# Kernel tuning notes

Hardware: AMD Instinct MI355X
Metric: run time of the kernel (lower is better)

## Reference

```python
import jax, jax.numpy as jnp
import numpy as np

B, S, HID = 1, 2048, 1024
HQ, HKV, D = 16, 8, 64
W = 64          # causal window size (includes self at offset 0)
K = 128         # total neighbors per query: W window + (K-W) random rewires


def setup_inputs() -> dict:
    key = jax.random.key(0)
    ks = jax.random.split(key, 8)
    hidden_states = jax.random.normal(ks[0], (B, S, HID), jnp.float32)
    sc = HID ** -0.5
    q_w = jax.random.normal(ks[1], (HQ * D, HID), jnp.float32) * sc
    k_w = jax.random.normal(ks[2], (HKV * D, HID), jnp.float32) * sc
    v_w = jax.random.normal(ks[3], (HKV * D, HID), jnp.float32) * sc
    o_w = jax.random.normal(ks[4], (HQ * D, HID), jnp.float32).T * sc  # [HID, HQ*D] -> stored as [HID, HQ*D]? keep [HID, HQ*D]
    o_w = jax.random.normal(ks[4], (HID, HQ * D), jnp.float32) * sc
    edge_bias = jax.random.normal(ks[5], (4,), jnp.float32) * 0.1
    # neighbor indices: per kv-head, per query position.
    pos = jnp.arange(S)
    win = pos[:, None] - jnp.arange(W)[None, :]                    # [S, W], offset 0 == self
    win = jnp.broadcast_to(win[None], (HKV, S, W))
    rew = jax.random.randint(ks[6], (HKV, S, K - W), 0, S)         # random rewire edges
    neigh_idx = jnp.concatenate([win, rew], axis=-1).astype(jnp.int32)  # [HKV, S, K]
    edge_type = jnp.concatenate([
        jnp.full((HKV, S, W), 1, jnp.int32),       # 'window'
        jnp.full((HKV, S, K - W), 3, jnp.int32),   # 'rewire'
    ], axis=-1)
    return {
        'hidden_states': hidden_states, 'q_w': q_w, 'k_w': k_w, 'v_w': v_w,
        'o_w': o_w, 'edge_bias': edge_bias, 'neigh_idx': neigh_idx,
        'edge_type': edge_type,
    }


def reference(hidden_states, q_w, k_w, v_w, o_w, edge_bias, neigh_idx, edge_type):
    b, s, _ = hidden_states.shape
    hkv, _, kk = neigh_idx.shape
    hq = q_w.shape[0] // (k_w.shape[0] // hkv)
    d = k_w.shape[0] // hkv
    hq = q_w.shape[0] // d
    g = hq // hkv
    scaling = d ** -0.5

    # projections (nn.Linear: x @ W.T)
    q = (hidden_states @ q_w.T).reshape(b, s, hq, d).transpose(0, 2, 1, 3)    # [B,HQ,S,D]
    k = (hidden_states @ k_w.T).reshape(b, s, hkv, d).transpose(0, 2, 1, 3)   # [B,HKV,S,D]
    v = (hidden_states @ v_w.T).reshape(b, s, hkv, d).transpose(0, 2, 1, 3)

    # causal neighbor mask + safe clamp (mirrors _causal_neighbor_mask / _safe_neighbor_idx)
    pos = jnp.arange(s)
    mask = (neigh_idx >= 0) & (neigh_idx < s) & (neigh_idx <= pos[None, :, None])  # [HKV,S,K]
    safe = jnp.clip(neigh_idx, 0, s - 1)

    # gather K/V at neighbor indices: [B,HKV,S,K,D]
    h_idx = jnp.arange(hkv)[:, None, None]
    k_g = k[:, h_idx, safe, :]
    v_g = v[:, h_idx, safe, :]

    # GQA: group query heads over kv heads
    qg = q.reshape(b, hkv, g, s, d)
    scores = jnp.einsum('bhgsd,bhskd->bhgsk', qg, k_g) * scaling              # [B,HKV,G,S,K]
    scores = scores + edge_bias[edge_type][None, :, None, :, :]
    neg = jnp.finfo(scores.dtype).min
    scores = jnp.where(mask[None, :, None, :, :], scores, neg)
    attn = jax.nn.softmax(scores, axis=-1)

    out = jnp.einsum('bhgsk,bhskd->bhgsd', attn, v_g)                         # [B,HKV,G,S,D]
    out = out.reshape(b, hq, s, d).transpose(0, 2, 1, 3).reshape(b, s, hq * d)
    return out @ o_w.T                                                        # [B,S,HID]
```

## Files before the change

kernel.cpp:

```cpp
#include <hip/hip_runtime.h>
#include <hip/hip_bf16.h>

#define S_LEN 2048
#define HIDDEN 1024

typedef __attribute__((ext_vector_type(4))) float f32x4;
typedef __attribute__((ext_vector_type(8))) _Float16 f16x8;
typedef __attribute__((ext_vector_type(2))) _Float16 f16x2;
typedef __attribute__((ext_vector_type(2))) __fp16 fp16x2;
typedef unsigned short u16;
typedef unsigned int u32;

typedef const __attribute__((address_space(1))) unsigned int as1_u32;
typedef __attribute__((address_space(3))) unsigned int as3_u32;

__device__ __forceinline__ u16 f2h(float f) {
  union { _Float16 h; u16 u; } c; c.h = (_Float16)f; return c.u;
}
__device__ __forceinline__ f16x2 u2h2(u32 u) {
  union { u32 x; f16x2 h; } c; c.x = u; return c.h;
}
__device__ __forceinline__ float fdot2(u32 a, u32 b, float c) {
#if __has_builtin(__builtin_amdgcn_fdot2)
  return __builtin_amdgcn_fdot2(u2h2(a), u2h2(b), c, false);
#else
  f16x2 ha = u2h2(a), hb = u2h2(b);
  return fmaf((float)ha.x, (float)hb.x, fmaf((float)ha.y, (float)hb.y, c));
#endif
}
__device__ __forceinline__ u32 pkrtz(float a, float b) {
#if __has_builtin(__builtin_amdgcn_cvt_pkrtz)
  union { fp16x2 h; u32 u; } c;
  c.h = __builtin_amdgcn_cvt_pkrtz(a, b);
  return c.u;
#else
  union { f16x2 h; u32 u; } c;
  c.h.x = (_Float16)a; c.h.y = (_Float16)b;
  return c.u;
#endif
}
__device__ __forceinline__ u32 alignbit16(u32 hi, u32 lo) {
#if __has_builtin(__builtin_amdgcn_alignbit)
  return __builtin_amdgcn_alignbit(hi, lo, 16);
#else
  return (hi << 16) | (lo >> 16);
#endif
}

__global__ __launch_bounds__(256) void cvt_all(
    const float* __restrict__ h, const float* __restrict__ qw,
    const float* __restrict__ kw, const float* __restrict__ vw,
    const float* __restrict__ ow, u16* __restrict__ hb, u16* __restrict__ qwb,
    u16* __restrict__ kwb, u16* __restrict__ vwb, u16* __restrict__ owb) {
  const int b = blockIdx.x;
  const float* src; u16* dst; int base;
  if (b < 2048)      { src = h;  dst = hb;  base = b; }
  else if (b < 3072) { src = qw; dst = qwb; base = b - 2048; }
  else if (b < 3584) { src = kw; dst = kwb; base = b - 3072; }
  else if (b < 4096) { src = vw; dst = vwb; base = b - 3584; }
  else               { src = ow; dst = owb; base = b - 4096; }
  const int i = base * 256 + threadIdx.x;
  const float4 v = ((const float4*)src)[i];
  ushort4 r;
  r.x = f2h(v.x); r.y = f2h(v.y); r.z = f2h(v.z); r.w = f2h(v.w);
  ((ushort4*)dst)[i] = r;
}

template <int BM, bool OUT_F16>
__device__ __forceinline__ void gemm_core(
    u16* __restrict__ As, u16* __restrict__ Bs,
    const u16* __restrict__ A, const u16* __restrict__ W, void* __restrict__ Cv,
    int Kd, int ldc, int mtile, int ntile) {
  constexpr int MF = BM / 32;
  const int tid = threadIdx.x;
  const int lane = tid & 63;
  const int wave = tid >> 6;
  const int wr = wave >> 1, wc = wave & 1;
  f32x4 acc[MF][4] = {};
  const int m0 = mtile * BM, n0 = ntile * 128;
  const int nk = Kd >> 5;

  auto stage = [&](int buf, int kt) {
    u16* Ad = As + buf * (BM * 32);
    u16* Bd = Bs + buf * (128 * 32);
#pragma unroll
    for (int i = 0; i < BM / 64; ++i) {
      const int e = (i * 256 + tid) * 8;
      const int r = e >> 5, c = e & 31;
      __builtin_amdgcn_global_load_lds(
          (as1_u32*)(A + (size_t)(m0 + r) * Kd + kt * 32 + c), (as3_u32*)(Ad + e), 16, 0, 0);
    }
#pragma unroll
    for (int i = 0; i < 2; ++i) {
      const int e = (i * 256 + tid) * 8;
      const int r = e >> 5, c = e & 31;
      __builtin_amdgcn_global_load_lds(
          (as1_u32*)(W + (size_t)(n0 + r) * Kd + kt * 32 + c), (as3_u32*)(Bd + e), 16, 0, 0);
    }
  };

  stage(0, 0);
  __syncthreads();
  int cur = 0;
  for (int kt = 0; kt < nk; ++kt) {
    if (kt + 1 < nk) stage(cur ^ 1, kt + 1);
    const u16* Ac = As + cur * (BM * 32);
    const u16* Bc = Bs + cur * (128 * 32);
    f16x8 af[MF], bfr[4];
#pragma unroll
    for (int mi = 0; mi < MF; ++mi)
      af[mi] = *(const f16x8*)(Ac + (wr * (BM / 2) + mi * 16 + (lane & 15)) * 32 + (lane >> 4) * 8);
#pragma unroll
    for (int ni = 0; ni < 4; ++ni)
      bfr[ni] = *(const f16x8*)(Bc + (wc * 64 + ni * 16 + (lane & 15)) * 32 + (lane >> 4) * 8);
#pragma unroll
    for (int mi = 0; mi < MF; ++mi)
#pragma unroll
      for (int ni = 0; ni < 4; ++ni)
        acc[mi][ni] = __builtin_amdgcn_mfma_f32_16x16x32_f16(af[mi], bfr[ni], acc[mi][ni], 0, 0, 0);
    __syncthreads();
    cur ^= 1;
  }

#pragma unroll
  for (int mi = 0; mi < MF; ++mi) {
#pragma unroll
    for (int ni = 0; ni < 4; ++ni) {
      const int row0 = m0 + wr * (BM / 2) + mi * 16 + (lane >> 4) * 4;
      const int col = n0 + wc * 64 + ni * 16 + (lane & 15);
#pragma unroll
      for (int r = 0; r < 4; ++r) {
        if (OUT_F16)
          ((u16*)Cv)[(size_t)(row0 + r) * ldc + col] = f2h(acc[mi][ni][r]);
        else
          ((float*)Cv)[(size_t)(row0 + r) * ldc + col] = acc[mi][ni][r];
      }
    }
  }
}

__global__ __launch_bounds__(256, 2) void qkv_gemm(
    const u16* __restrict__ hb, const u16* __restrict__ qwb,
    const u16* __restrict__ kwb, const u16* __restrict__ vwb,
    u16* __restrict__ Qb, u16* __restrict__ Kb, u16* __restrict__ Vb) {
  __shared__ u16 As[2 * 128 * 32];
  __shared__ u16 Bs[2 * 128 * 32];
  const int nt = blockIdx.x, mt = blockIdx.y;
  if (nt < 8)       gemm_core<128, true>(As, Bs, hb, qwb, Qb, HIDDEN, 1024, mt, nt);
  else if (nt < 12) gemm_core<128, true>(As, Bs, hb, kwb, Kb, HIDDEN, 512, mt, nt - 8);
  else              gemm_core<128, true>(As, Bs, hb, vwb, Vb, HIDDEN, 512, mt, nt - 12);
}

__global__ __launch_bounds__(256, 2) void o_gemm(
    const u16* __restrict__ attnb, const u16* __restrict__ owb,
    float* __restrict__ out) {
  __shared__ u16 As[2 * 64 * 32];
  __shared__ u16 Bs[2 * 128 * 32];
  gemm_core<64, false>(As, Bs, attnb, owb, out, HIDDEN, 1024, blockIdx.y, blockIdx.x);
}

#define WIN_ROWS 72
#define WIN_ELEMS (WIN_ROWS * 64)
#define VT_LD 41
__global__ __launch_bounds__(256) void attn_kernel(
    const u16* __restrict__ Qb, const u16* __restrict__ Kb,
    const u16* __restrict__ Vb, const int* __restrict__ neigh,
    const float* __restrict__ ebias, u16* __restrict__ attnb) {
  __shared__ u16 kwin[WIN_ELEMS];
  __shared__ u32 vwinT[64 * VT_LD];
  __shared__ u32 park[4][192];

  const int tid = threadIdx.x;
  const int lane = tid & 63;
  const int wv = tid >> 6;
  const int h = blockIdx.y;
  const int s0 = blockIdx.x * 4;
  const int s = s0 + wv;

  const u16* Kp = Kb + h * 64;
  const u16* Vp = Vb + h * 64;

  const int iB = neigh[((size_t)h * S_LEN + s) * 128 + 64 + lane];
  const bool okB = (iB >= 0) && (iB <= s);
  const int gB = min(max(iB, 0), S_LEN - 1);
  const bool okA = lane <= s;

  const u16* krp = Kp + (size_t)gB * 512;
  uint4 krreg[8];
#pragma unroll
  for (int t = 0; t < 8; ++t) krreg[t] = *(const uint4*)(krp + t * 8);

  const int chunk = (lane & 7) ^ (lane >> 3);
#pragma unroll
  for (int gg = 0; gg < 2; ++gg) {
    const int g = wv + gg * 4;
    const int r_lds = g * 8 + (lane >> 3);
    const int row = min(max(s0 - 63 + r_lds, 0), S_LEN - 1);
    __builtin_amdgcn_global_load_lds(
        (as1_u32*)(Kp + (size_t)row * 512 + chunk * 8),
        (as3_u32*)(kwin + g * 512 + lane * 8), 16, 0, 0);
  }
  if (wv == 0) {
    const int g = 8;
    const int r_lds = g * 8 + (lane >> 3);
    const int row = min(max(s0 - 63 + r_lds, 0), S_LEN - 1);
    __builtin_amdgcn_global_load_lds(
        (as1_u32*)(Kp + (size_t)row * 512 + chunk * 8),
        (as3_u32*)(kwin + g * 512 + lane * 8), 16, 0, 0);
  }

#pragma unroll 3
  for (int t = 0; t < 9; ++t) {
    const int k = wv + 4 * t;
    const int i0r = 2 * k;
    const int g0 = min(max(s0 - 63 + i0r, 0), S_LEN - 1);
    const int g1 = min(max(s0 - 62 + i0r, 0), S_LEN - 1);
    const u32 w0 = Vp[(size_t)g0 * 512 + lane];
    const u32 w1 = Vp[(size_t)g1 * 512 + lane];
    vwinT[lane * VT_LD + k] = (w1 << 16) | w0;
  }

  __syncthreads();

  const u16* qp = Qb + (size_t)s * 1024 + h * 128;
  const int rW = wv + 63 - lane;
  const u16* kwrow = kwin + rW * 64;
  const int rw7 = rW & 7;
  float sA0 = 0.f, sA1 = 0.f, sB0 = 0.f, sB1 = 0.f;
#pragma unroll
  for (int t = 0; t < 8; ++t) {
    const uint4 kw = *(const uint4*)(kwrow + ((t ^ rw7) << 3));
    const uint4 kr = krreg[t];
    const uint4 qa = *(const uint4*)(qp + t * 8);
    const uint4 qb = *(const uint4*)(qp + 64 + t * 8);
    sA0 = fdot2(kw.x, qa.x, sA0); sA0 = fdot2(kw.y, qa.y, sA0);
    sA0 = fdot2(kw.z, qa.z, sA0); sA0 = fdot2(kw.w, qa.w, sA0);
    sA1 = fdot2(kw.x, qb.x, sA1); sA1 = fdot2(kw.y, qb.y, sA1);
    sA1 = fdot2(kw.z, qb.z, sA1); sA1 = fdot2(kw.w, qb.w, sA1);
    sB0 = fdot2(kr.x, qa.x, sB0); sB0 = fdot2(kr.y, qa.y, sB0);
    sB0 = fdot2(kr.z, qa.z, sB0); sB0 = fdot2(kr.w, qa.w, sB0);
    sB1 = fdot2(kr.x, qb.x, sB1); sB1 = fdot2(kr.y, qb.y, sB1);
    sB1 = fdot2(kr.z, qb.z, sB1); sB1 = fdot2(kr.w, qb.w, sB1);
  }

  const float NEG = -1e30f;
  const float SC = 0.125f;
  const float ebW = ebias[1];
  const float ebR = ebias[3];
  sA0 = okA ? fmaf(sA0, SC, ebW) : NEG;
  sA1 = okA ? fmaf(sA1, SC, ebW) : NEG;
  sB0 = okB ? fmaf(sB0, SC, ebR) : NEG;
  sB1 = okB ? fmaf(sB1, SC, ebR) : NEG;

  float m0 = fmaxf(sA0, sB0), m1 = fmaxf(sA1, sB1);
#pragma unroll
  for (int off = 32; off; off >>= 1) {
    m0 = fmaxf(m0, __shfl_xor(m0, off));
    m1 = fmaxf(m1, __shfl_xor(m1, off));
  }
  float eA0 = __expf(sA0 - m0), eB0 = __expf(sB0 - m0);
  float eA1 = __expf(sA1 - m1), eB1 = __expf(sB1 - m1);
  float d0 = eA0 + eB0, d1 = eA1 + eB1;
#pragma unroll
  for (int off = 32; off; off >>= 1) {
    d0 += __shfl_xor(d0, off);
    d1 += __shfl_xor(d1, off);
  }
  const float rc0 = 1.0f / d0, rc1 = 1.0f / d1;

  u32* pb = park[wv];
  int* ib = (int*)(park[wv] + 128);
  const float pA0 = eA0 * rc0, pA1 = eA1 * rc1;
  const float pB0 = eB0 * rc0, pB1 = eB1 * rc1;
  const float hA0 = __shfl_xor(pA0, 1), hA1 = __shfl_xor(pA1, 1);
  const float hB0 = __shfl_xor(pB0, 1), hB1 = __shfl_xor(pB1, 1);
  ib[lane] = gB;
  if (!(lane & 1)) {
    uint4 pk;
    pk.x = pkrtz(hA0, pA0);
    pk.y = pkrtz(hA1, pA1);
    pk.z = pkrtz(pB0, hB0);
    pk.w = pkrtz(pB1, hB1);
    *(uint4*)(pb + (lane >> 1) * 4) = pk;
  }
  asm volatile("s_waitcnt lgkmcnt(0)" ::: "memory");

  float a0 = 0.f, a1 = 0.f;
  const u32* vtr = vwinT + lane * VT_LD;
  const int keven = (wv >> 1) + 31;
  const int kodd = ((wv + 63) >> 1);
#pragma unroll 4
  for (int m = 0; m < 32; ++m) {
    const uint4 pp = *(const uint4*)(pb + m * 4);
    const int2 rB = *(const int2*)(ib + m * 2);
    u32 wpair;
    if ((wv & 1) == 0) {
      wpair = vtr[keven - m];
    } else {
      const u32 lo = vtr[kodd - 1 - m];
      const u32 hi = vtr[kodd - m];
      wpair = alignbit16(hi, lo);
    }
    const u32 b0 = Vp[(size_t)rB.x * 512 + lane];
    const u32 b1 = Vp[(size_t)rB.y * 512 + lane];
    const u32 bpair = (b1 << 16) | b0;
    a0 = fdot2(wpair, pp.x, a0);
    a1 = fdot2(wpair, pp.y, a1);
    a0 = fdot2(bpair, pp.z, a0);
    a1 = fdot2(bpair, pp.w, a1);
  }

  u16* op = attnb + (size_t)s * 1024 + h * 128;
  op[lane] = f2h(a0);
  op[64 + lane] = f2h(a1);
}

extern "C" void kernel_launch(void* const* d_in, const int* in_sizes, int n_in,
                              void* d_out, int out_size, void* d_ws, size_t ws_size,
                              hipStream_t stream) {
  const float* hidden = (const float*)d_in[0];
  const float* q_w = (const float*)d_in[1];
  const float* k_w = (const float*)d_in[2];
  const float* v_w = (const float*)d_in[3];
  const float* o_w = (const float*)d_in[4];
  const float* ebias = (const float*)d_in[5];
  const int* neigh = (const int*)d_in[6];
  float* out = (float*)d_out;

  char* ws = (char*)d_ws;
  u16* hb    = (u16*)(ws + (0ull << 20));
  u16* qwb   = (u16*)(ws + (4ull << 20));
  u16* kwb   = (u16*)(ws + (6ull << 20));
  u16* vwb   = (u16*)(ws + (7ull << 20));
  u16* owb   = (u16*)(ws + (8ull << 20));
  u16* Qb    = (u16*)(ws + (10ull << 20));
  u16* Kb    = (u16*)(ws + (14ull << 20));
  u16* Vb    = (u16*)(ws + (16ull << 20));
  u16* attnb = (u16*)(ws + (18ull << 20));

  cvt_all<<<5120, 256, 0, stream>>>(hidden, q_w, k_w, v_w, o_w,
                                    hb, qwb, kwb, vwb, owb);
  qkv_gemm<<<dim3(16, 16), 256, 0, stream>>>(hb, qwb, kwb, vwb, Qb, Kb, Vb);
  attn_kernel<<<dim3(512, 8), 256, 0, stream>>>(Qb, Kb, Vb, neigh, ebias, attnb);
  o_gemm<<<dim3(8, 32), 256, 0, stream>>>(attnb, owb, out);
}
```

Measured before the change: 95.48 us.

## Drop LDS window staging in attention; read window K/V directly from global

```diff
diff --git a/kernel.cpp b/kernel.cpp
--- a/kernel.cpp
+++ b/kernel.cpp
@@ -37,13 +37,6 @@
   union { f16x2 h; u32 u; } c;
   c.h.x = (_Float16)a; c.h.y = (_Float16)b;
   return c.u;
-#endif
-}
-__device__ __forceinline__ u32 alignbit16(u32 hi, u32 lo) {
-#if __has_builtin(__builtin_amdgcn_alignbit)
-  return __builtin_amdgcn_alignbit(hi, lo, 16);
-#else
-  return (hi << 16) | (lo >> 16);
 #endif
 }
 
@@ -159,78 +152,35 @@
   gemm_core<64, false>(As, Bs, attnb, owb, out, HIDDEN, 1024, blockIdx.y, blockIdx.x);
 }
 
-#define WIN_ROWS 72
-#define WIN_ELEMS (WIN_ROWS * 64)
-#define VT_LD 41
 __global__ __launch_bounds__(256) void attn_kernel(
     const u16* __restrict__ Qb, const u16* __restrict__ Kb,
     const u16* __restrict__ Vb, const int* __restrict__ neigh,
     const float* __restrict__ ebias, u16* __restrict__ attnb) {
-  __shared__ u16 kwin[WIN_ELEMS];
-  __shared__ u32 vwinT[64 * VT_LD];
   __shared__ u32 park[4][192];
 
   const int tid = threadIdx.x;
   const int lane = tid & 63;
   const int wv = tid >> 6;
   const int h = blockIdx.y;
-  const int s0 = blockIdx.x * 4;
-  const int s = s0 + wv;
+  const int su = __builtin_amdgcn_readfirstlane(blockIdx.x * 4 + wv);
 
   const u16* Kp = Kb + h * 64;
   const u16* Vp = Vb + h * 64;
 
-  const int iB = neigh[((size_t)h * S_LEN + s) * 128 + 64 + lane];
-  const bool okB = (iB >= 0) && (iB <= s);
+  const int iB = neigh[((size_t)h * S_LEN + su) * 128 + 64 + lane];
+  const bool okB = (iB >= 0) && (iB <= su);
   const int gB = min(max(iB, 0), S_LEN - 1);
-  const bool okA = lane <= s;
-
+  const bool okA = lane <= su;
+  const int gA = max(su - lane, 0);
+
+  const u16* qp = Qb + (size_t)su * 1024 + h * 128;
+  const u16* kwp = Kp + (size_t)gA * 512;
   const u16* krp = Kp + (size_t)gB * 512;
-  uint4 krreg[8];
-#pragma unroll
-  for (int t = 0; t < 8; ++t) krreg[t] = *(const uint4*)(krp + t * 8);
-
-  const int chunk = (lane & 7) ^ (lane >> 3);
-#pragma unroll
-  for (int gg = 0; gg < 2; ++gg) {
-    const int g = wv + gg * 4;
-    const int r_lds = g * 8 + (lane >> 3);
-    const int row = min(max(s0 - 63 + r_lds, 0), S_LEN - 1);
-    __builtin_amdgcn_global_load_lds(
-        (as1_u32*)(Kp + (size_t)row * 512 + chunk * 8),
-        (as3_u32*)(kwin + g * 512 + lane * 8), 16, 0, 0);
-  }
-  if (wv == 0) {
-    const int g = 8;
-    const int r_lds = g * 8 + (lane >> 3);
-    const int row = min(max(s0 - 63 + r_lds, 0), S_LEN - 1);
-    __builtin_amdgcn_global_load_lds(
-        (as1_u32*)(Kp + (size_t)row * 512 + chunk * 8),
-        (as3_u32*)(kwin + g * 512 + lane * 8), 16, 0, 0);
-  }
-
-#pragma unroll 3
-  for (int t = 0; t < 9; ++t) {
-    const int k = wv + 4 * t;
-    const int i0r = 2 * k;
-    const int g0 = min(max(s0 - 63 + i0r, 0), S_LEN - 1);
-    const int g1 = min(max(s0 - 62 + i0r, 0), S_LEN - 1);
-    const u32 w0 = Vp[(size_t)g0 * 512 + lane];
-    const u32 w1 = Vp[(size_t)g1 * 512 + lane];
-    vwinT[lane * VT_LD + k] = (w1 << 16) | w0;
-  }
-
-  __syncthreads();
-
-  const u16* qp = Qb + (size_t)s * 1024 + h * 128;
-  const int rW = wv + 63 - lane;
-  const u16* kwrow = kwin + rW * 64;
-  const int rw7 = rW & 7;
   float sA0 = 0.f, sA1 = 0.f, sB0 = 0.f, sB1 = 0.f;
 #pragma unroll
   for (int t = 0; t < 8; ++t) {
-    const uint4 kw = *(const uint4*)(kwrow + ((t ^ rw7) << 3));
-    const uint4 kr = krreg[t];
+    const uint4 kw = *(const uint4*)(kwp + t * 8);
+    const uint4 kr = *(const uint4*)(krp + t * 8);
     const uint4 qa = *(const uint4*)(qp + t * 8);
     const uint4 qb = *(const uint4*)(qp + 64 + t * 8);
     sA0 = fdot2(kw.x, qa.x, sA0); sA0 = fdot2(kw.y, qa.y, sA0);
@@ -277,8 +227,8 @@
   ib[lane] = gB;
   if (!(lane & 1)) {
     uint4 pk;
-    pk.x = pkrtz(hA0, pA0);
-    pk.y = pkrtz(hA1, pA1);
+    pk.x = pkrtz(pA0, hA0);
+    pk.y = pkrtz(pA1, hA1);
     pk.z = pkrtz(pB0, hB0);
     pk.w = pkrtz(pB1, hB1);
     *(uint4*)(pb + (lane >> 1) * 4) = pk;
@@ -286,23 +236,17 @@
   asm volatile("s_waitcnt lgkmcnt(0)" ::: "memory");
 
   float a0 = 0.f, a1 = 0.f;
-  const u32* vtr = vwinT + lane * VT_LD;
-  const int keven = (wv >> 1) + 31;
-  const int kodd = ((wv + 63) >> 1);
 #pragma unroll 4
   for (int m = 0; m < 32; ++m) {
     const uint4 pp = *(const uint4*)(pb + m * 4);
     const int2 rB = *(const int2*)(ib + m * 2);
-    u32 wpair;
-    if ((wv & 1) == 0) {
-      wpair = vtr[keven - m];
-    } else {
-      const u32 lo = vtr[kodd - 1 - m];
-      const u32 hi = vtr[kodd - m];
-      wpair = alignbit16(hi, lo);
-    }
+    const int r0w = max(su - 2 * m, 0);
+    const int r1w = max(su - 2 * m - 1, 0);
+    const u32 w0 = Vp[(size_t)r0w * 512 + lane];
+    const u32 w1 = Vp[(size_t)r1w * 512 + lane];
     const u32 b0 = Vp[(size_t)rB.x * 512 + lane];
     const u32 b1 = Vp[(size_t)rB.y * 512 + lane];
+    const u32 wpair = (w1 << 16) | w0;
     const u32 bpair = (b1 << 16) | b0;
     a0 = fdot2(wpair, pp.x, a0);
     a1 = fdot2(wpair, pp.y, a1);
@@ -310,7 +254,7 @@
     a1 = fdot2(bpair, pp.w, a1);
   }
 
-  u16* op = attnb + (size_t)s * 1024 + h * 128;
+  u16* op = attnb + (size_t)su * 1024 + h * 128;
   op[lane] = f2h(a0);
   op[64 + lane] = f2h(a1);
 }
```

Result: slower. 106.1 us (+11.1%).

## Stage random-neighbor K/V rows into LDS via async loads, 8 queries per block

Applied to the files above, without the earlier changes.

```diff
diff --git a/kernel.cpp b/kernel.cpp
--- a/kernel.cpp
+++ b/kernel.cpp
@@ -162,56 +162,70 @@
 #define WIN_ROWS 72
 #define WIN_ELEMS (WIN_ROWS * 64)
 #define VT_LD 41
-__global__ __launch_bounds__(256) void attn_kernel(
+__global__ __launch_bounds__(512) void attn_kernel(
     const u16* __restrict__ Qb, const u16* __restrict__ Kb,
     const u16* __restrict__ Vb, const int* __restrict__ neigh,
     const float* __restrict__ ebias, u16* __restrict__ attnb) {
   __shared__ u16 kwin[WIN_ELEMS];
   __shared__ u32 vwinT[64 * VT_LD];
-  __shared__ u32 park[4][192];
+  __shared__ u16 krand[8][4096];
+  __shared__ u16 vrand[8][4096];
 
   const int tid = threadIdx.x;
   const int lane = tid & 63;
   const int wv = tid >> 6;
   const int h = blockIdx.y;
-  const int s0 = blockIdx.x * 4;
-  const int s = s0 + wv;
+  const int s0 = blockIdx.x * 8;
+  const int su = __builtin_amdgcn_readfirstlane(s0 + wv);
 
   const u16* Kp = Kb + h * 64;
   const u16* Vp = Vb + h * 64;
 
-  const int iB = neigh[((size_t)h * S_LEN + s) * 128 + 64 + lane];
-  const bool okB = (iB >= 0) && (iB <= s);
+  const int iB = neigh[((size_t)h * S_LEN + su) * 128 + 64 + lane];
+  const bool okB = (iB >= 0) && (iB <= su);
   const int gB = min(max(iB, 0), S_LEN - 1);
-  const bool okA = lane <= s;
-
-  const u16* krp = Kp + (size_t)gB * 512;
-  uint4 krreg[8];
-#pragma unroll
-  for (int t = 0; t < 8; ++t) krreg[t] = *(const uint4*)(krp + t * 8);
-
+  const bool okA = lane <= su;
+
+  u16* krw = krand[wv];
+  u16* vrw = vrand[wv];
   const int chunk = (lane & 7) ^ (lane >> 3);
-#pragma unroll
-  for (int gg = 0; gg < 2; ++gg) {
-    const int g = wv + gg * 4;
-    const int r_lds = g * 8 + (lane >> 3);
-    const int row = min(max(s0 - 63 + r_lds, 0), S_LEN - 1);
+
+  {
+    int g = wv;
+    int r_lds = g * 8 + (lane >> 3);
+    int row = min(max(s0 - 63 + r_lds, 0), S_LEN - 1);
     __builtin_amdgcn_global_load_lds(
         (as1_u32*)(Kp + (size_t)row * 512 + chunk * 8),
         (as3_u32*)(kwin + g * 512 + lane * 8), 16, 0, 0);
-  }
-  if (wv == 0) {
-    const int g = 8;
-    const int r_lds = g * 8 + (lane >> 3);
-    const int row = min(max(s0 - 63 + r_lds, 0), S_LEN - 1);
+    if (wv == 0) {
+      g = 8;
+      r_lds = g * 8 + (lane >> 3);
+      row = min(max(s0 - 63 + r_lds, 0), S_LEN - 1);
+      __builtin_amdgcn_global_load_lds(
+          (as1_u32*)(Kp + (size_t)row * 512 + chunk * 8),
+          (as3_u32*)(kwin + g * 512 + lane * 8), 16, 0, 0);
+    }
+  }
+
+#pragma unroll
+  for (int g2 = 0; g2 < 8; ++g2) {
+    const int row = __shfl(gB, g2 * 8 + (lane >> 3));
     __builtin_amdgcn_global_load_lds(
         (as1_u32*)(Kp + (size_t)row * 512 + chunk * 8),
-        (as3_u32*)(kwin + g * 512 + lane * 8), 16, 0, 0);
-  }
-
-#pragma unroll 3
-  for (int t = 0; t < 9; ++t) {
-    const int k = wv + 4 * t;
+        (as3_u32*)(krw + g2 * 512 + lane * 8), 16, 0, 0);
+  }
+
+#pragma unroll
+  for (int g2 = 0; g2 < 8; ++g2) {
+    const int row = __shfl(gB, g2 * 8 + (lane >> 3));
+    __builtin_amdgcn_global_load_lds(
+        (as1_u32*)(Vp + (size_t)row * 512 + (lane & 7) * 8),
+        (as3_u32*)(vrw + g2 * 512 + lane * 8), 16, 0, 0);
+  }
+
+#pragma unroll
+  for (int t = 0; t < 5; ++t) {
+    const int k = wv + 8 * t;
     const int i0r = 2 * k;
     const int g0 = min(max(s0 - 63 + i0r, 0), S_LEN - 1);
     const int g1 = min(max(s0 - 62 + i0r, 0), S_LEN - 1);
@@ -222,15 +236,16 @@
 
   __syncthreads();
 
-  const u16* qp = Qb + (size_t)s * 1024 + h * 128;
+  const u16* qp = Qb + (size_t)su * 1024 + h * 128;
   const int rW = wv + 63 - lane;
   const u16* kwrow = kwin + rW * 64;
-  const int rw7 = rW & 7;
+  const u16* krrow = krw + lane * 64;
+  const int rw7 = rW & 7, ln7 = lane & 7;
   float sA0 = 0.f, sA1 = 0.f, sB0 = 0.f, sB1 = 0.f;
 #pragma unroll
   for (int t = 0; t < 8; ++t) {
     const uint4 kw = *(const uint4*)(kwrow + ((t ^ rw7) << 3));
-    const uint4 kr = krreg[t];
+    const uint4 kr = *(const uint4*)(krrow + ((t ^ ln7) << 3));
     const uint4 qa = *(const uint4*)(qp + t * 8);
     const uint4 qb = *(const uint4*)(qp + 64 + t * 8);
     sA0 = fdot2(kw.x, qa.x, sA0); sA0 = fdot2(kw.y, qa.y, sA0);
@@ -268,13 +283,12 @@
   }
   const float rc0 = 1.0f / d0, rc1 = 1.0f / d1;
 
-  u32* pb = park[wv];
-  int* ib = (int*)(park[wv] + 128);
+  asm volatile("s_waitcnt lgkmcnt(0)" ::: "memory");
+  u32* pb = (u32*)krw;
   const float pA0 = eA0 * rc0, pA1 = eA1 * rc1;
   const float pB0 = eB0 * rc0, pB1 = eB1 * rc1;
   const float hA0 = __shfl_xor(pA0, 1), hA1 = __shfl_xor(pA1, 1);
   const float hB0 = __shfl_xor(pB0, 1), hB1 = __shfl_xor(pB1, 1);
-  ib[lane] = gB;
   if (!(lane & 1)) {
     uint4 pk;
     pk.x = pkrtz(hA0, pA0);
@@ -288,11 +302,10 @@
   float a0 = 0.f, a1 = 0.f;
   const u32* vtr = vwinT + lane * VT_LD;
   const int keven = (wv >> 1) + 31;
-  const int kodd = ((wv + 63) >> 1);
+  const int kodd = (wv + 63) >> 1;
 #pragma unroll 4
   for (int m = 0; m < 32; ++m) {
     const uint4 pp = *(const uint4*)(pb + m * 4);
-    const int2 rB = *(const int2*)(ib + m * 2);
     u32 wpair;
     if ((wv & 1) == 0) {
       wpair = vtr[keven - m];
@@ -301,8 +314,8 @@
       const u32 hi = vtr[kodd - m];
       wpair = alignbit16(hi, lo);
     }
-    const u32 b0 = Vp[(size_t)rB.x * 512 + lane];
-    const u32 b1 = Vp[(size_t)rB.y * 512 + lane];
+    const u32 b0 = vrw[(2 * m) * 64 + lane];
+    const u32 b1 = vrw[(2 * m + 1) * 64 + lane];
     const u32 bpair = (b1 << 16) | b0;
     a0 = fdot2(wpair, pp.x, a0);
     a1 = fdot2(wpair, pp.y, a1);
@@ -310,7 +323,7 @@
     a1 = fdot2(bpair, pp.w, a1);
   }
 
-  u16* op = attnb + (size_t)s * 1024 + h * 128;
+  u16* op = attnb + (size_t)su * 1024 + h * 128;
   op[lane] = f2h(a0);
   op[64 + lane] = f2h(a1);
 }
@@ -341,6 +354,6 @@
   cvt_all<<<5120, 256, 0, stream>>>(hidden, q_w, k_w, v_w, o_w,
                                     hb, qwb, kwb, vwb, owb);
   qkv_gemm<<<dim3(16, 16), 256, 0, stream>>>(hb, qwb, kwb, vwb, Qb, Kb, Vb);
-  attn_kernel<<<dim3(512, 8), 256, 0, stream>>>(Qb, Kb, Vb, neigh, ebias, attnb);
+  attn_kernel<<<dim3(256, 8), 512, 0, stream>>>(Qb, Kb, Vb, neigh, ebias, attnb);
   o_gemm<<<dim3(8, 32), 256, 0, stream>>>(attnb, owb, out);
 }
```

After: 111.3 us. 16.6% more time.
